# Optimization experiments

Measured on AMD Instinct MI355X. Metric: run time of the kernel, lower is better.

The kernel has to match this reference:

```python
import jax, jax.numpy as jnp
import numpy as np

PROX_TOL = 5
SEG_PENALTY = 3.0
SEG_REWARD = 0.3
CLASS_WEIGHTS = np.array([0.1, 5.0, 5.0], dtype=np.float32)


def setup_inputs() -> dict:
    key = jax.random.key(0)
    k1, k2, k3 = jax.random.split(key, 3)
    B, S, C = 256, 16384, 3
    logits = jax.random.normal(k1, (B, S, C), dtype=jnp.float32)
    labels = jax.random.randint(k2, (B, S), 0, 3, dtype=jnp.int64)
    tokens = jax.random.randint(k3, (B, S), 0, 1000, dtype=jnp.int64)
    return {"logits": logits, "labels": labels, "tokens": tokens}


def _window_any(mask, tol):
    # sliding 'any' over [t-tol, t+tol], clipped at sequence edges ('SAME' padding)
    m = mask.astype(jnp.float32)
    r = jax.lax.reduce_window(m, 0.0, jax.lax.max, (1, 2 * tol + 1), (1, 1), 'SAME')
    return r > 0.0


def reference(logits, labels, tokens):
    B, S, C = logits.shape
    cw = jnp.asarray(CLASS_WEIGHTS, dtype=logits.dtype)

    # weighted cross-entropy, reduction='none' -> w[y] * nll  [B, S]
    logp = jax.nn.log_softmax(logits, axis=-1)
    nll = -jnp.take_along_axis(logp, labels[..., None], axis=-1)[..., 0]
    base_loss = nll * cw[labels]

    predictions = jnp.argmax(logits, axis=-1)
    pred_switch = predictions >= 1   # [B, S]
    true_switch = labels >= 1        # [B, S]

    # segmentation adjustment (tokens is not None): for predicted switches,
    # the t+1 < S check overwrites the penalty with the reward, so:
    #   t <  S-1        -> reward
    #   t == S-1, t>=1  -> penalty (offset loop fired)
    pos = jnp.arange(S)
    adj = jnp.where(pred_switch & (pos < S - 1), SEG_REWARD,
                    jnp.where(pred_switch & (pos == S - 1) & (pos >= 1), SEG_PENALTY, 1.0))
    base_loss = base_loss * adj.astype(base_loss.dtype)

    # proximity reward: true switch with any predicted switch within +/- tol -> *0.1
    pred_near = _window_any(pred_switch, PROX_TOL)
    base_loss = jnp.where(true_switch & pred_near, base_loss * 0.1, base_loss)

    # false-positive penalty: predicted switch farther than tol from every true
    # switch -> *2.0 (only applied if the sequence has at least one true switch)
    true_near = _window_any(true_switch, PROX_TOL)
    has_true = jnp.any(true_switch, axis=1, keepdims=True)
    base_loss = jnp.where(pred_switch & has_true & (~true_near), base_loss * 2.0, base_loss)

    valid_mask = (labels != -100).astype(base_loss.dtype)
    return (base_loss * valid_mask).sum() / valid_mask.sum()
```

## Files before the change

### kernel.cpp

```cpp
#include <hip/hip_runtime.h>

#define SEQ 16384
#define TOL 5
#define CHUNK 2048
#define NCHUNK (SEQ / CHUNK)
#define NW (CHUNK / 64)
#define P 8
#define NROW 256
#define NBLK (NROW * NCHUNK)
#define TOTAL_VALID 4194304.0


__global__ __launch_bounds__(256, 4) void switch_loss_kernel(
    const float* __restrict__ logits,
    const int* __restrict__ labels,
    float* __restrict__ blk_sum, float* __restrict__ blk_fp,
    int* __restrict__ blk_any)
{
    const int row = blockIdx.y;
    const int chunk = blockIdx.x;
    const int s0 = chunk * CHUNK;
    const int t = threadIdx.x;
    const int w = t >> 6;
    const int lane = t & 63;

    __shared__ unsigned long long ps[NW + 2];
    __shared__ unsigned long long ts[NW + 2];
    __shared__ __align__(8) unsigned char psb[256];
    __shared__ __align__(8) unsigned char tsb[256];
    __shared__ float wsum[4], wfp[4];
    __shared__ int wany[4];

    const float* __restrict__ lrow = logits + (size_t)row * (SEQ * 3);
    const int* __restrict__ labrow = labels + (size_t)row * SEQ;

    const int sb = s0 + t * P;

    const float4* __restrict__ lp = (const float4*)(lrow + (size_t)sb * 3);
    const float4 f0 = lp[0], f1 = lp[1], f2 = lp[2], f3 = lp[3], f4 = lp[4], f5 = lp[5];
    const int4* __restrict__ yp = (const int4*)(labrow + sb);
    const int4 ya = yp[0], yb = yp[1];

    bool hp = false, ht = false;
    if (t < 2 * TOL) {
        const int pos = (t < TOL) ? (s0 - TOL + t) : (s0 + CHUNK + (t - TOL));
        if (pos >= 0 && pos < SEQ) {
            const float h0 = lrow[pos * 3 + 0];
            const float h1 = lrow[pos * 3 + 1];
            const float h2 = lrow[pos * 3 + 2];
            hp = (h1 > h0) || (h2 > fmaxf(h0, h1));
            ht = (labrow[pos] >= 1);
        }
    }
    if (w == 0) {
        const unsigned long long bp = __ballot(hp);
        const unsigned long long bt = __ballot(ht);
        if (lane == 0) {
            ps[0] = (bp & 0x1Full) << 59;
            ts[0] = (bt & 0x1Full) << 59;
            ps[NW + 1] = (bp >> TOL) & 0x1Full;
            ts[NW + 1] = (bt >> TOL) & 0x1Full;
        }
    }

    const float L0[P] = {f0.x, f0.w, f1.z, f2.y, f3.x, f3.w, f4.z, f5.y};
    const float L1[P] = {f0.y, f1.x, f1.w, f2.z, f3.y, f4.x, f4.w, f5.z};
    const float L2[P] = {f0.z, f1.y, f2.x, f2.w, f3.z, f4.y, f5.x, f5.w};
    const int   Y[P]  = {ya.x, ya.y, ya.z, ya.w, yb.x, yb.y, yb.z, yb.w};

    float lossv[P];
    unsigned pn = 0, tn = 0;
    #pragma unroll
    for (int p = 0; p < P; ++p) {
        const float l0 = L0[p], l1 = L1[p], l2 = L2[p];
        const int y = Y[p];

        const float m01 = fmaxf(l0, l1);
        const float mx = fmaxf(m01, l2);
        const bool psw = (l1 > l0) || (l2 > m01);

        const float sum = __expf(l0 - mx) + __expf(l1 - mx) + __expf(l2 - mx);
        const float lse = mx + __logf(sum);

        const bool valid = (y >= 0) && (y <= 2);
        const bool tsw = valid && (y >= 1);
        const float ly = (y == 0) ? l0 : ((y == 1) ? l1 : l2);
        const float wgt = (y == 0) ? 0.1f : 5.0f;
        float loss = valid ? (lse - ly) * wgt : 0.0f;

        const int s = sb + p;
        const float adj = psw ? ((s < SEQ - 1) ? 0.3f : 3.0f) : 1.0f;
        lossv[p] = loss * adj;

        pn |= (unsigned)psw << p;
        tn |= (unsigned)tsw << p;
    }
    psb[t] = (unsigned char)pn;
    tsb[t] = (unsigned char)tn;
    {
        const unsigned long long ba = __ballot(tn != 0);
        if (lane == 0) wany[w] = (ba != 0ull) ? 1 : 0;
    }
    __syncthreads();

    if (t < NW) {
        ps[1 + t] = *(const unsigned long long*)&psb[t * 8];
        ts[1 + t] = *(const unsigned long long*)&tsb[t * 8];
    }
    __syncthreads();

    float lsum = 0.0f, lfp = 0.0f;
    #pragma unroll
    for (int p = 0; p < P; ++p) {
        const int s = sb + p;
        const bool psw = (pn >> p) & 1u;
        const bool tsw = (tn >> p) & 1u;

        int lo = s - TOL; lo = (lo < 0) ? 0 : lo;
        int hi = s + TOL; hi = (hi > SEQ - 1) ? (SEQ - 1) : hi;
        const int len = hi - lo + 1;
        const int rel = lo - s0 + 64;
        const int qq = rel >> 6;
        const int sh = rel & 63;

        unsigned long long pw = ps[qq] >> sh;
        unsigned long long tw = ts[qq] >> sh;
        if (sh + len > 64) {
            pw |= ps[qq + 1] << (64 - sh);
            tw |= ts[qq + 1] << (64 - sh);
        }
        const unsigned long long mlen = (1ull << len) - 1ull;
        const bool pred_near = (pw & mlen) != 0ull;
        const bool true_near = (tw & mlen) != 0ull;

        float loss = lossv[p];
        if (tsw && pred_near) loss *= 0.1f;
        lsum += loss;
        if (psw && !true_near) lfp += loss;
    }

    #pragma unroll
    for (int off = 32; off > 0; off >>= 1) {
        lsum += __shfl_down(lsum, off, 64);
        lfp  += __shfl_down(lfp, off, 64);
    }
    if (lane == 0) { wsum[w] = lsum; wfp[w] = lfp; }
    __syncthreads();
    if (t == 0) {
        const int slot = row * NCHUNK + chunk;
        blk_sum[slot] = wsum[0] + wsum[1] + wsum[2] + wsum[3];
        blk_fp[slot]  = wfp[0] + wfp[1] + wfp[2] + wfp[3];
        blk_any[slot] = wany[0] | wany[1] | wany[2] | wany[3];
    }
}

__global__ void finalize_kernel(const float* __restrict__ blk_sum,
                                const float* __restrict__ blk_fp,
                                const int* __restrict__ blk_any,
                                float* __restrict__ out) {
    const int t = threadIdx.x;
    const int w = t >> 6, lane = t & 63;
    __shared__ double wsumd[4];

    const float4* __restrict__ fs = (const float4*)(blk_sum + t * NCHUNK);
    const float4* __restrict__ ff = (const float4*)(blk_fp + t * NCHUNK);
    const int4* __restrict__ fa = (const int4*)(blk_any + t * NCHUNK);
    const float4 s0v = fs[0], s1v = fs[1];
    const float4 f0v = ff[0], f1v = ff[1];
    const int4 a0 = fa[0], a1 = fa[1];

    const float s = ((s0v.x + s0v.y) + (s0v.z + s0v.w)) + ((s1v.x + s1v.y) + (s1v.z + s1v.w));
    const float f = ((f0v.x + f0v.y) + (f0v.z + f0v.w)) + ((f1v.x + f1v.y) + (f1v.z + f1v.w));
    const int any = a0.x | a0.y | a0.z | a0.w | a1.x | a1.y | a1.z | a1.w;

    double v = (double)s + (any ? (double)f : 0.0);
    #pragma unroll
    for (int off = 32; off > 0; off >>= 1)
        v += __shfl_down(v, off, 64);
    if (lane == 0) wsumd[w] = v;
    __syncthreads();
    if (t == 0)
        out[0] = (float)((wsumd[0] + wsumd[1] + wsumd[2] + wsumd[3]) / TOTAL_VALID);
}

extern "C" void kernel_launch(void* const* d_in, const int* in_sizes, int n_in,
                              void* d_out, int out_size, void* d_ws, size_t ws_size,
                              hipStream_t stream) {
    const float* logits = (const float*)d_in[0];
    const int* labels = (const int*)d_in[1];
    (void)in_sizes; (void)n_in; (void)out_size; (void)ws_size;

    float* blk_sum = (float*)d_ws;
    float* blk_fp = blk_sum + NBLK;
    int* blk_any = (int*)(blk_fp + NBLK);
    float* out = (float*)d_out;

    switch_loss_kernel<<<dim3(NCHUNK, NROW), 256, 0, stream>>>(
        logits, labels, blk_sum, blk_fp, blk_any);
    finalize_kernel<<<1, 256, 0, stream>>>(blk_sum, blk_fp, blk_any, out);
}
```

Baseline: 109.4 us.

## Fuse finalize into main kernel via last-block atomic counters

Result: slower. 181.7 us (+66.1%).

```diff
diff --git a/kernel.cpp b/kernel.cpp
--- a/kernel.cpp
+++ b/kernel.cpp
@@ -10,12 +10,15 @@
 #define NBLK (NROW * NCHUNK)
 #define TOTAL_VALID 4194304.0
 
+#define CNT_OFF (NBLK*4*3 + NROW*8)
+#define CNT_BYTES (NROW*4 + 4)
 
 __global__ __launch_bounds__(256, 4) void switch_loss_kernel(
     const float* __restrict__ logits,
     const int* __restrict__ labels,
-    float* __restrict__ blk_sum, float* __restrict__ blk_fp,
-    int* __restrict__ blk_any)
+    float* blk_sum, float* blk_fp, int* blk_any,
+    double* row_total, int* rowcnt, int* gcnt,
+    float* __restrict__ out)
 {
     const int row = blockIdx.y;
     const int chunk = blockIdx.x;
@@ -30,6 +33,10 @@
     __shared__ __align__(8) unsigned char tsb[256];
     __shared__ float wsum[4], wfp[4];
     __shared__ int wany[4];
+    __shared__ int rowlast_s, glast_s;
+    __shared__ float ss[NCHUNK], sf[NCHUNK];
+    __shared__ int sa[NCHUNK];
+    __shared__ double wsumd[4];
 
     const float* __restrict__ lrow = logits + (size_t)row * (SEQ * 3);
     const int* __restrict__ labrow = labels + (size_t)row * SEQ;
@@ -146,41 +153,47 @@
     }
     if (lane == 0) { wsum[w] = lsum; wfp[w] = lfp; }
     __syncthreads();
+
     if (t == 0) {
         const int slot = row * NCHUNK + chunk;
         blk_sum[slot] = wsum[0] + wsum[1] + wsum[2] + wsum[3];
         blk_fp[slot]  = wfp[0] + wfp[1] + wfp[2] + wfp[3];
         blk_any[slot] = wany[0] | wany[1] | wany[2] | wany[3];
-    }
-}
-
-__global__ void finalize_kernel(const float* __restrict__ blk_sum,
-                                const float* __restrict__ blk_fp,
-                                const int* __restrict__ blk_any,
-                                float* __restrict__ out) {
-    const int t = threadIdx.x;
-    const int w = t >> 6, lane = t & 63;
-    __shared__ double wsumd[4];
-
-    const float4* __restrict__ fs = (const float4*)(blk_sum + t * NCHUNK);
-    const float4* __restrict__ ff = (const float4*)(blk_fp + t * NCHUNK);
-    const int4* __restrict__ fa = (const int4*)(blk_any + t * NCHUNK);
-    const float4 s0v = fs[0], s1v = fs[1];
-    const float4 f0v = ff[0], f1v = ff[1];
-    const int4 a0 = fa[0], a1 = fa[1];
-
-    const float s = ((s0v.x + s0v.y) + (s0v.z + s0v.w)) + ((s1v.x + s1v.y) + (s1v.z + s1v.w));
-    const float f = ((f0v.x + f0v.y) + (f0v.z + f0v.w)) + ((f1v.x + f1v.y) + (f1v.z + f1v.w));
-    const int any = a0.x | a0.y | a0.z | a0.w | a1.x | a1.y | a1.z | a1.w;
-
-    double v = (double)s + (any ? (double)f : 0.0);
-    #pragma unroll
-    for (int off = 32; off > 0; off >>= 1)
-        v += __shfl_down(v, off, 64);
-    if (lane == 0) wsumd[w] = v;
-    __syncthreads();
-    if (t == 0)
-        out[0] = (float)((wsumd[0] + wsumd[1] + wsumd[2] + wsumd[3]) / TOTAL_VALID);
+        __threadfence();
+        const int old = atomicAdd(rowcnt + row, 1);
+        rowlast_s = (old == NCHUNK - 1);
+    }
+    __syncthreads();
+
+    if (rowlast_s) {
+        if (t < NCHUNK) {
+            ss[t] = atomicAdd(blk_sum + row * NCHUNK + t, 0.0f);
+            sf[t] = atomicAdd(blk_fp + row * NCHUNK + t, 0.0f);
+            sa[t] = atomicOr(blk_any + row * NCHUNK + t, 0);
+        }
+        __syncthreads();
+        if (t == 0) {
+            float s = 0.0f, f = 0.0f; int a = 0;
+            #pragma unroll
+            for (int c = 0; c < NCHUNK; ++c) { s += ss[c]; f += sf[c]; a |= sa[c]; }
+            row_total[row] = (double)s + (a ? (double)f : 0.0);
+            __threadfence();
+            const int old = atomicAdd(gcnt, 1);
+            glast_s = (old == NROW - 1);
+        }
+        __syncthreads();
+
+        if (glast_s) {
+            double v = atomicAdd(row_total + t, 0.0);
+            #pragma unroll
+            for (int off = 32; off > 0; off >>= 1)
+                v += __shfl_down(v, off, 64);
+            if (lane == 0) wsumd[w] = v;
+            __syncthreads();
+            if (t == 0)
+                out[0] = (float)((wsumd[0] + wsumd[1] + wsumd[2] + wsumd[3]) / TOTAL_VALID);
+        }
+    }
 }
 
 extern "C" void kernel_launch(void* const* d_in, const int* in_sizes, int n_in,
@@ -190,12 +203,17 @@
     const int* labels = (const int*)d_in[1];
     (void)in_sizes; (void)n_in; (void)out_size; (void)ws_size;
 
-    float* blk_sum = (float*)d_ws;
+    char* ws = (char*)d_ws;
+    float* blk_sum = (float*)ws;
     float* blk_fp = blk_sum + NBLK;
     int* blk_any = (int*)(blk_fp + NBLK);
+    double* row_total = (double*)(blk_any + NBLK);
+    int* rowcnt = (int*)(ws + CNT_OFF);
+    int* gcnt = rowcnt + NROW;
     float* out = (float*)d_out;
 
+    hipMemsetAsync(ws + CNT_OFF, 0, CNT_BYTES, stream);
+
     switch_loss_kernel<<<dim3(NCHUNK, NROW), 256, 0, stream>>>(
-        logits, labels, blk_sum, blk_fp, blk_any);
-    finalize_kernel<<<1, 256, 0, stream>>>(blk_sum, blk_fp, blk_any, out);
+        logits, labels, blk_sum, blk_fp, blk_any, row_total, rowcnt, gcnt, out);
 }
```
